# Performance work log

Measured on AMD Instinct MI355X. Metric: run time of the kernel, lower is better.

## Reference

```python
import jax, jax.numpy as jnp
import numpy as np

EMBED_DIM = 64   # conv out channels / linear in features
PATCH_DIM = 64   # linear out features
KSIZE, STRIDE, PAD = 5, 2, 2
B, T = 4, 480000


def setup_inputs() -> dict:
    key = jax.random.key(0)
    k1, k2, k3, k4, k5 = jax.random.split(key, 5)
    audio_waveform = jax.random.normal(k1, (B, T), jnp.float32)
    # conv1d weights: [out_ch, in_ch, k]
    conv_w = jax.random.normal(k2, (EMBED_DIM, 1, KSIZE), jnp.float32) / np.sqrt(KSIZE).astype(np.float32)
    conv_b = 0.01 * jax.random.normal(k3, (EMBED_DIM,), jnp.float32)
    # linear patch encoder: [patch_dim, embed_dim] (torch convention W @ x)
    lin_w = jax.random.normal(k4, (PATCH_DIM, EMBED_DIM), jnp.float32) / np.sqrt(EMBED_DIM).astype(np.float32)
    lin_b = 0.01 * jax.random.normal(k5, (PATCH_DIM,), jnp.float32)
    return dict(audio_waveform=audio_waveform, conv_w=conv_w, conv_b=conv_b,
                lin_w=lin_w, lin_b=lin_b)


def reference(audio_waveform, conv_w, conv_b, lin_w, lin_b):
    # [B, T] -> [B, 1, T]
    x = audio_waveform[:, None, :]
    # Conv1d(1 -> EMBED_DIM, k=5, stride=2, pad=2): [B, E, T//2]
    feats = jax.lax.conv_general_dilated(
        x, conv_w, window_strides=(STRIDE,), padding=[(PAD, PAD)],
        dimension_numbers=('NCH', 'OIH', 'NCH'))
    feats = jax.nn.relu(feats + conv_b[None, :, None])
    feats = feats.transpose(0, 2, 1)  # [B, seq_len, E]
    # Per-timestep linear patch encoder. NOTE: the torch module's
    # entropy-gated segmentation loop only chooses patch boundaries;
    # since patches are re-concatenated in order and the Linear is
    # applied per timestep, the output is exactly this, for any
    # entropy predictor / threshold.
    return jnp.einsum('bse,pe->bsp', feats, lin_w) + lin_b
```

## Files before the change

### kernel.cpp

```cpp
#include <hip/hip_runtime.h>
#include <hip/hip_bf16.h>
#include <stdint.h>

#define B_SZ    4
#define T_LEN   480000
#define S_LEN   240000
#define KS      5
#define TPB     15000
#define NTILES  (B_SZ * TPB)
#define GRID    512

typedef __attribute__((ext_vector_type(8))) __bf16  bf16x8;
typedef __attribute__((ext_vector_type(4))) float   f32x4;

__global__ __launch_bounds__(256) void audio_enc_kernel(
    const float* __restrict__ audio,
    const float* __restrict__ conv_w,
    const float* __restrict__ conv_b,
    const float* __restrict__ lin_w,
    const float* __restrict__ lin_b,
    float* __restrict__ out)
{
  const int lane = threadIdx.x & 63;
  const int m    = lane & 15;
  const int q    = lane >> 4;
  const int wv   = (blockIdx.x << 2) | (threadIdx.x >> 6);
  const int nw   = gridDim.x << 2;

  float cw[2][8][KS], cbv[2][8];
#pragma unroll
  for (int h = 0; h < 2; ++h)
#pragma unroll
    for (int j = 0; j < 8; ++j) {
      const int e = h * 32 + q * 8 + j;
#pragma unroll
      for (int t = 0; t < KS; ++t) cw[h][j][t] = conv_w[e * KS + t];
      cbv[h][j] = conv_b[e];
    }

  bf16x8 bfrag[2][4];
#pragma unroll
  for (int nt = 0; nt < 4; ++nt) {
    const int p = nt * 16 + m;
#pragma unroll
    for (int kt = 0; kt < 2; ++kt) {
      const float* src = lin_w + p * 64 + kt * 32 + q * 8;
#pragma unroll
      for (int j = 0; j < 8; ++j) bfrag[kt][nt][j] = (__bf16)src[j];
    }
  }
  float lbv[4];
#pragma unroll
  for (int nt = 0; nt < 4; ++nt) lbv[nt] = lin_b[nt * 16 + m];

  int t = wv;
  if (t >= NTILES) return;

  auto load_tile = [&](int tt, float2& A, float2& B, float& C) {
    const unsigned ut = (unsigned)tt;
    const unsigned b  = ut / TPB;
    const int s0      = (int)(ut - b * TPB) * 16;
    const int sl      = s0 + m;
    const float* base = audio + (size_t)b * T_LEN;
    const int gi = 2 * sl - 2;
    A = *reinterpret_cast<const float2*>(base + (gi < 0 ? 0 : gi));
    if (gi < 0) { A.x = 0.f; A.y = 0.f; }
    B = *reinterpret_cast<const float2*>(base + 2 * sl);
    const int ci = 2 * sl + 2;
    float cv = base[ci < T_LEN ? ci : T_LEN - 1];
    C = (ci < T_LEN) ? cv : 0.f;
  };

  float2 fa, fb; float c1;
  load_tile(t, fa, fb, c1);

  while (true) {
    const float x0 = fa.x, x1 = fa.y, x2 = fb.x, x3 = fb.y, x4 = c1;
    const unsigned ut = (unsigned)t;
    const unsigned b  = ut / TPB;
    const int s0      = (int)(ut - b * TPB) * 16;

    const int tn = t + nw;
    const bool more = (tn < NTILES);
    if (more) load_tile(tn, fa, fb, c1);

    bf16x8 af[2];
#pragma unroll
    for (int h = 0; h < 2; ++h)
#pragma unroll
      for (int j = 0; j < 8; ++j) {
        float a = cbv[h][j];
        a = fmaf(cw[h][j][0], x0, a);
        a = fmaf(cw[h][j][1], x1, a);
        a = fmaf(cw[h][j][2], x2, a);
        a = fmaf(cw[h][j][3], x3, a);
        a = fmaf(cw[h][j][4], x4, a);
        a = fmaxf(a, 0.f);
        af[h][j] = (__bf16)a;
      }

    float* ob = out + ((size_t)b * S_LEN + (size_t)s0) * 64;
#pragma unroll
    for (int nt = 0; nt < 4; ++nt) {
      f32x4 acc = {0.f, 0.f, 0.f, 0.f};
      acc = __builtin_amdgcn_mfma_f32_16x16x32_bf16(af[0], bfrag[0][nt], acc, 0, 0, 0);
      acc = __builtin_amdgcn_mfma_f32_16x16x32_bf16(af[1], bfrag[1][nt], acc, 0, 0, 0);
      const float bias = lbv[nt];
#pragma unroll
      for (int r = 0; r < 4; ++r) {
        ob[(q * 4 + r) * 64 + nt * 16 + m] = acc[r] + bias;
      }
    }

    if (!more) break;
    t = tn;
  }
}

extern "C" void kernel_launch(void* const* d_in, const int* in_sizes, int n_in,
                              void* d_out, int out_size, void* d_ws, size_t ws_size,
                              hipStream_t stream) {
  const float* audio  = (const float*)d_in[0];
  const float* conv_w = (const float*)d_in[1];
  const float* conv_b = (const float*)d_in[2];
  const float* lin_w  = (const float*)d_in[3];
  const float* lin_b  = (const float*)d_in[4];
  float* out = (float*)d_out;

  audio_enc_kernel<<<dim3(GRID), dim3(256), 0, stream>>>(
      audio, conv_w, conv_b, lin_w, lin_b, out);
}
```

Measured before the change: 274.4 us.

## Swap MFMA operands for vectorized float4 output stores, fold bias, raise grid

Swaps the MFMA A/B operands so each lane holds four consecutive output features of one timestep. Those can then be written as a single 16-byte store instead of four scattered scalar stores. The linear bias is preloaded as the accumulator init, and the per-tile integer division is replaced by incremental batch/offset advance. The grid is tripled to raise occupancy for this store-bound kernel, at the cost of a static assumption that the wave stride never exceeds a batch.

Result: slower. 291.0 us (+6.0%).

```diff
diff --git a/kernel.cpp b/kernel.cpp
--- a/kernel.cpp
+++ b/kernel.cpp
@@ -8,7 +8,9 @@
 #define KS      5
 #define TPB     15000
 #define NTILES  (B_SZ * TPB)
-#define GRID    512
+#define GRID    1536
+
+static_assert(4 * GRID <= TPB, "single-wrap batch advance requires nw <= TPB");
 
 typedef __attribute__((ext_vector_type(8))) __bf16  bf16x8;
 typedef __attribute__((ext_vector_type(4))) float   f32x4;
@@ -24,8 +26,8 @@
   const int lane = threadIdx.x & 63;
   const int m    = lane & 15;
   const int q    = lane >> 4;
-  const int wv   = (blockIdx.x << 2) | (threadIdx.x >> 6);
-  const int nw   = gridDim.x << 2;
+  const int wv   = (int)((blockIdx.x << 2) | (threadIdx.x >> 6));
+  const int nw   = (int)(gridDim.x << 2);
 
   float cw[2][8][KS], cbv[2][8];
 #pragma unroll
@@ -38,7 +40,7 @@
       cbv[h][j] = conv_b[e];
     }
 
-  bf16x8 bfrag[2][4];
+  bf16x8 wfrag[2][4];
 #pragma unroll
   for (int nt = 0; nt < 4; ++nt) {
     const int p = nt * 16 + m;
@@ -46,45 +48,44 @@
     for (int kt = 0; kt < 2; ++kt) {
       const float* src = lin_w + p * 64 + kt * 32 + q * 8;
 #pragma unroll
-      for (int j = 0; j < 8; ++j) bfrag[kt][nt][j] = (__bf16)src[j];
+      for (int j = 0; j < 8; ++j) wfrag[kt][nt][j] = (__bf16)src[j];
     }
   }
-  float lbv[4];
+
+  f32x4 lb4[4];
 #pragma unroll
-  for (int nt = 0; nt < 4; ++nt) lbv[nt] = lin_b[nt * 16 + m];
+  for (int nt = 0; nt < 4; ++nt)
+    lb4[nt] = *reinterpret_cast<const f32x4*>(lin_b + nt * 16 + q * 4);
 
-  int t = wv;
-  if (t >= NTILES) return;
+  if (wv >= NTILES) return;
+  int b  = wv / TPB;
+  int sb = wv - b * TPB;
 
-  auto load_tile = [&](int tt, float2& A, float2& B, float& C) {
-    const unsigned ut = (unsigned)tt;
-    const unsigned b  = ut / TPB;
-    const int s0      = (int)(ut - b * TPB) * 16;
-    const int sl      = s0 + m;
-    const float* base = audio + (size_t)b * T_LEN;
+  auto load_tile = [&](int bb, int s0, float2& A, float2& Bv, float& C) {
+    const float* base = audio + (size_t)bb * T_LEN;
+    const int sl = s0 + m;
     const int gi = 2 * sl - 2;
     A = *reinterpret_cast<const float2*>(base + (gi < 0 ? 0 : gi));
     if (gi < 0) { A.x = 0.f; A.y = 0.f; }
-    B = *reinterpret_cast<const float2*>(base + 2 * sl);
+    Bv = *reinterpret_cast<const float2*>(base + 2 * sl);
     const int ci = 2 * sl + 2;
-    float cv = base[ci < T_LEN ? ci : T_LEN - 1];
+    const float cv = base[ci < T_LEN ? ci : T_LEN - 1];
     C = (ci < T_LEN) ? cv : 0.f;
   };
 
   float2 fa, fb; float c1;
-  load_tile(t, fa, fb, c1);
+  load_tile(b, sb * 16, fa, fb, c1);
 
   while (true) {
     const float x0 = fa.x, x1 = fa.y, x2 = fb.x, x3 = fb.y, x4 = c1;
-    const unsigned ut = (unsigned)t;
-    const unsigned b  = ut / TPB;
-    const int s0      = (int)(ut - b * TPB) * 16;
+    const int bc = b, s0 = sb * 16;
 
-    const int tn = t + nw;
-    const bool more = (tn < NTILES);
-    if (more) load_tile(tn, fa, fb, c1);
+    int sbn = sb + nw, bn = b;
+    if (sbn >= TPB) { sbn -= TPB; ++bn; }
+    const bool more = (bn < B_SZ);
+    if (more) load_tile(bn, sbn * 16, fa, fb, c1);
 
-    bf16x8 af[2];
+    bf16x8 xf[2];
 #pragma unroll
     for (int h = 0; h < 2; ++h)
 #pragma unroll
@@ -96,24 +97,20 @@
         a = fmaf(cw[h][j][3], x3, a);
         a = fmaf(cw[h][j][4], x4, a);
         a = fmaxf(a, 0.f);
-        af[h][j] = (__bf16)a;
+        xf[h][j] = (__bf16)a;
       }
 
-    float* ob = out + ((size_t)b * S_LEN + (size_t)s0) * 64;
+    float* op = out + ((size_t)bc * S_LEN + (size_t)s0 + m) * 64 + q * 4;
 #pragma unroll
     for (int nt = 0; nt < 4; ++nt) {
-      f32x4 acc = {0.f, 0.f, 0.f, 0.f};
-      acc = __builtin_amdgcn_mfma_f32_16x16x32_bf16(af[0], bfrag[0][nt], acc, 0, 0, 0);
-      acc = __builtin_amdgcn_mfma_f32_16x16x32_bf16(af[1], bfrag[1][nt], acc, 0, 0, 0);
-      const float bias = lbv[nt];
-#pragma unroll
-      for (int r = 0; r < 4; ++r) {
-        ob[(q * 4 + r) * 64 + nt * 16 + m] = acc[r] + bias;
-      }
+      f32x4 acc = lb4[nt];
+      acc = __builtin_amdgcn_mfma_f32_16x16x32_bf16(wfrag[0][nt], xf[0], acc, 0, 0, 0);
+      acc = __builtin_amdgcn_mfma_f32_16x16x32_bf16(wfrag[1][nt], xf[1], acc, 0, 0, 0);
+      *reinterpret_cast<f32x4*>(op + nt * 16) = acc;
     }
 
     if (!more) break;
-    t = tn;
+    b = bn; sb = sbn;
   }
 }
 
```
